# Performance work log

Hardware: AMD Instinct MI355X
Metric: run time of the kernel (lower is better)

The kernel has to match this reference:

```python
import jax, jax.numpy as jnp
from jax import lax
import numpy as np

V, H, D, B, W = 256, 512, 2, 256, 256  # vector_size, hidden_size, depth, batch, window_size


def setup_inputs() -> dict:
    key = jax.random.key(0)
    ks = jax.random.split(key, 13)
    scale = 0.04  # ~ 1/sqrt(hidden)
    names = ["w_ih_ltr", "w_hh_ltr", "b_ih_ltr", "b_hh_ltr", "w_fc_ltr", "b_fc_ltr",
             "w_ih_rtl", "w_hh_rtl", "b_ih_rtl", "b_hh_rtl", "w_fc_rtl", "b_fc_rtl"]
    shapes = [(D, 4 * H, V), (D, 4 * H, H), (D, 4 * H), (D, 4 * H), (D, V, H), (D, V)] * 2
    inp = {"x": jax.random.normal(ks[0], (B, W, V), dtype=jnp.float32)}
    for i, (n, s) in enumerate(zip(names, shapes)):
        inp[n] = jax.random.normal(ks[i + 1], s, dtype=jnp.float32) * scale
    return inp


def _lstm_cell(x, h, c, wih, whh, bih, bhh):
    # PyTorch gate order: i, f, g, o
    g = x @ wih.T + bih + h @ whh.T + bhh
    i, f, gg, o = jnp.split(g, 4, axis=-1)
    c = jax.nn.sigmoid(f) * c + jax.nn.sigmoid(i) * jnp.tanh(gg)
    h = jax.nn.sigmoid(o) * jnp.tanh(c)
    return h, c


def _run_dir(xs, wih, whh, bih, bhh, wfc, bfc):
    # xs: (T, B, V); depth LSTM(1-step)+FC blocks with persistent (h,c) per depth
    depth = wih.shape[0]
    h0 = jnp.zeros((depth, xs.shape[1], whh.shape[-1]), xs.dtype)

    def step(carry, x):
        h, c = carry
        v = x
        hs, cs = [], []
        for j in range(depth):  # small fixed depth loop
            hj, cj = _lstm_cell(v, h[j], c[j], wih[j], whh[j], bih[j], bhh[j])
            v = hj @ wfc[j].T + bfc[j]
            hs.append(hj)
            cs.append(cj)
        return (jnp.stack(hs), jnp.stack(cs)), v

    _, ys = lax.scan(step, (h0, h0), xs)
    return ys  # (T, B, V)


def reference(x, w_ih_ltr, w_hh_ltr, b_ih_ltr, b_hh_ltr, w_fc_ltr, b_fc_ltr,
              w_ih_rtl, w_hh_rtl, b_ih_rtl, b_hh_rtl, w_fc_rtl, b_fc_rtl):
    Wlen = x.shape[1]
    xs_f = jnp.swapaxes(x[:, :Wlen - 1, :], 0, 1)        # steps i = 0 .. W-2
    xs_b = jnp.swapaxes(x[:, Wlen - 1:0:-1, :], 0, 1)    # steps -(i+1) = W-1 .. 1
    ys_f = _run_dir(xs_f, w_ih_ltr, w_hh_ltr, b_ih_ltr, b_hh_ltr, w_fc_ltr, b_fc_ltr)
    ys_b = _run_dir(xs_b, w_ih_rtl, w_hh_rtl, b_ih_rtl, b_hh_rtl, w_fc_rtl, b_fc_rtl)
    # torch.stack(output, dim=1): forward outputs then backward outputs -> (B, 2*(W-1), V)
    return jnp.swapaxes(jnp.concatenate([ys_f, ys_b], axis=0), 0, 1)
```

## Files before the change

### kernel.cpp

```cpp
#include <hip/hip_runtime.h>
#include <hip/hip_bf16.h>

using bf16   = __bf16;
using bf16x8 = __attribute__((ext_vector_type(8))) __bf16;
using f32x4  = __attribute__((ext_vector_type(4))) float;
using u32x4  = __attribute__((ext_vector_type(4))) unsigned int;

#define TSTEPS 255
#define UNITE  512
#define HPAR   (16*16*512)
#define WA_UNITS_DIR (128*24)
#define WB_UNITS_DIR (128*32)
#define WC_UNITS_DIR (16*16)

#define MFMA(acc, a, b) acc = __builtin_amdgcn_mfma_f32_16x16x32_bf16((a), (b), (acc), 0, 0, 0)

__device__ __forceinline__ float sigmoidf_(float x) { return 1.f / (1.f + __expf(-x)); }
__device__ __forceinline__ float tanhf_(float x) {
    float e = __expf(-2.f * fabsf(x));
    float t = (1.f - e) / (1.f + e);
    return copysignf(t, x);
}

__device__ __forceinline__ void storeh_coh(bf16* ph, bf16* pl,
                                           unsigned short vh, unsigned short vl) {
    asm volatile(
        "global_store_short %0, %2, off sc0 sc1\n\t"
        "global_store_short %1, %3, off sc0 sc1"
        :: "v"(ph), "v"(pl), "v"(vh), "v"(vl)
        : "memory");
}

__device__ __forceinline__ void stage32k_512(const bf16* gh, const bf16* gl,
                                             bf16* lds, int tid) {
    u32x4 a0, a1, b0, b1;
    const bf16* p0 = gh + tid * 8;
    const bf16* p1 = p0 + 4096;
    const bf16* q0 = gl + tid * 8;
    const bf16* q1 = q0 + 4096;
    asm volatile(
        "global_load_dwordx4 %0, %4, off sc0 sc1\n\t"
        "global_load_dwordx4 %1, %5, off sc0 sc1\n\t"
        "global_load_dwordx4 %2, %6, off sc0 sc1\n\t"
        "global_load_dwordx4 %3, %7, off sc0 sc1\n\t"
        "s_waitcnt vmcnt(0)"
        : "=&v"(a0), "=&v"(a1), "=&v"(b0), "=&v"(b1)
        : "v"(p0), "v"(p1), "v"(q0), "v"(q1)
        : "memory");
    *(u32x4*)(lds + tid * 8)               = a0;
    *(u32x4*)(lds + tid * 8 + 4096)        = a1;
    *(u32x4*)(lds + 8192 + tid * 8)        = b0;
    *(u32x4*)(lds + 8192 + tid * 8 + 4096) = b1;
}

__device__ __forceinline__ void split_store8(const float* __restrict__ src,
                                             bf16* __restrict__ dh, bf16* __restrict__ dl) {
    float f[8];
    *(float4*)f       = *(const float4*)src;
    *(float4*)(f + 4) = *(const float4*)(src + 4);
    bf16x8 oh, ol;
    #pragma unroll
    for (int j = 0; j < 8; ++j) { bf16 h = (bf16)f[j]; oh[j] = h; ol[j] = (bf16)(f[j] - (float)h); }
    *(bf16x8*)dh = oh; *(bf16x8*)dl = ol;
}

__device__ __forceinline__ void gbarrier(unsigned* __restrict__ flags, int bid, unsigned epoch) {
    asm volatile("s_waitcnt vmcnt(0)" ::: "memory");
    __syncthreads();
    if (threadIdx.x == 0)
        asm volatile("global_store_dword %0, %1, off sc0 sc1"
                     :: "v"(&flags[bid]), "v"(epoch) : "memory");
    if (threadIdx.x < 64) {
        const int l = threadIdx.x;
        for (;;) {
            unsigned f0 = __hip_atomic_load(&flags[l],       __ATOMIC_RELAXED, __HIP_MEMORY_SCOPE_AGENT);
            unsigned f1 = __hip_atomic_load(&flags[l + 64],  __ATOMIC_RELAXED, __HIP_MEMORY_SCOPE_AGENT);
            unsigned f2 = __hip_atomic_load(&flags[l + 128], __ATOMIC_RELAXED, __HIP_MEMORY_SCOPE_AGENT);
            unsigned f3 = __hip_atomic_load(&flags[l + 192], __ATOMIC_RELAXED, __HIP_MEMORY_SCOPE_AGENT);
            if (__all(f0 >= epoch && f1 >= epoch && f2 >= epoch && f3 >= epoch)) break;
            __builtin_amdgcn_s_sleep(1);
        }
    }
    __syncthreads();
}


__global__ void k_pack_wa(const float* __restrict__ wihL, const float* __restrict__ whhL,
                          const float* __restrict__ wihR, const float* __restrict__ whhR,
                          bf16* __restrict__ wah, bf16* __restrict__ wal) {
    int gid = blockIdx.x * 256 + threadIdx.x;
    int lane = gid & 63, u = gid >> 6;
    int kb = u % 24; int tn = (u / 24) & 127; int dir = u / 3072;
    int r = lane & 15, q = lane >> 4;
    int n = tn * 16 + r, k = kb * 32 + q * 8;
    const float* wih = dir ? wihR : wihL;
    const float* whh = dir ? whhR : whhL;
    const float* src = (k < 256) ? (wih + (size_t)n * 256 + k)
                                 : (whh + (size_t)n * 512 + (k - 256));
    split_store8(src, wah + (size_t)u * UNITE + lane * 8, wal + (size_t)u * UNITE + lane * 8);
}

__global__ void k_wcomb(const float* __restrict__ wihL, const float* __restrict__ wfcL,
                        const float* __restrict__ wihR, const float* __restrict__ wfcR,
                        float* __restrict__ wcf) {
    size_t gid = (size_t)blockIdx.x * 256 + threadIdx.x;
    int k = gid & 511; int n = (gid >> 9) & 2047; int dir = (int)(gid >> 20);
    const float* wih1 = (dir ? wihR : wihL) + (size_t)2048 * 256;
    const float* wfc0 = (dir ? wfcR : wfcL);
    float s = 0.f;
    #pragma unroll 8
    for (int v = 0; v < 256; ++v)
        s = fmaf(wih1[(size_t)n * 256 + v], wfc0[(size_t)v * 512 + k], s);
    wcf[gid] = s;
}

__global__ void k_pack_wb(const float* __restrict__ whhL, const float* __restrict__ whhR,
                          const float* __restrict__ wcf,
                          bf16* __restrict__ wbh, bf16* __restrict__ wbl) {
    int gid = blockIdx.x * 256 + threadIdx.x;
    int lane = gid & 63, u = gid >> 6;
    int kb = u & 31, tn = (u >> 5) & 127, dir = u >> 12;
    int r = lane & 15, q = lane >> 4;
    int n = tn * 16 + r, k = kb * 32 + q * 8;
    const float* src;
    if (k < 512) {
        src = wcf + ((size_t)dir * 2048 + n) * 512 + k;
    } else {
        const float* whh1 = (dir ? whhR : whhL) + (size_t)2048 * 512;
        src = whh1 + (size_t)n * 512 + (k - 512);
    }
    split_store8(src, wbh + (size_t)u * UNITE + lane * 8, wbl + (size_t)u * UNITE + lane * 8);
}

__global__ void k_pack_wc(const float* __restrict__ wfcL, const float* __restrict__ wfcR,
                          bf16* __restrict__ wch, bf16* __restrict__ wcl) {
    int gid = blockIdx.x * 256 + threadIdx.x;
    int lane = gid & 63, u = gid >> 6;
    int kb = u & 15, tn = (u >> 4) & 15, dir = u >> 8;
    int r = lane & 15, q = lane >> 4;
    int n = tn * 16 + r, k = kb * 32 + q * 8;
    const float* wfc1 = (dir ? wfcR : wfcL) + (size_t)256 * 512;
    split_store8(wfc1 + (size_t)n * 512 + k,
                 wch + (size_t)u * UNITE + lane * 8, wcl + (size_t)u * UNITE + lane * 8);
}

__global__ void k_bias(const float* __restrict__ bihL, const float* __restrict__ bhhL,
                       const float* __restrict__ bfcL, const float* __restrict__ wihL,
                       const float* __restrict__ bihR, const float* __restrict__ bhhR,
                       const float* __restrict__ bfcR, const float* __restrict__ wihR,
                       float* __restrict__ ba, float* __restrict__ bb, float* __restrict__ bc) {
    int gid = blockIdx.x * 256 + threadIdx.x;
    int n = gid & 2047, dir = gid >> 11;
    const float* bih = dir ? bihR : bihL;
    const float* bhh = dir ? bhhR : bhhL;
    const float* bfc = dir ? bfcR : bfcL;
    const float* wih1 = (dir ? wihR : wihL) + (size_t)2048 * 256;
    ba[dir * 2048 + n] = bih[n] + bhh[n];
    float s = bih[2048 + n] + bhh[2048 + n];
    #pragma unroll 8
    for (int v = 0; v < 256; ++v)
        s = fmaf(bfc[v], wih1[(size_t)n * 256 + v], s);
    bb[dir * 2048 + n] = s;
    if (n < 256) bc[dir * 256 + n] = bfc[256 + n];
}

__global__ __launch_bounds__(512) void bilstm_main(
    const float* __restrict__ x,
    const bf16* __restrict__ wah, const bf16* __restrict__ wal,
    const bf16* __restrict__ wbh, const bf16* __restrict__ wbl,
    const bf16* __restrict__ wch, const bf16* __restrict__ wcl,
    bf16* __restrict__ h0pk, bf16* __restrict__ h1pk,
    const float* __restrict__ ba, const float* __restrict__ bb,
    const float* __restrict__ bc, float* __restrict__ out,
    unsigned* __restrict__ flags)
{
    const int bid  = blockIdx.x;
    const int nslc = bid & 7;
    const int bq   = (bid >> 3) & 15;
    const int dir  = bid >> 7;
    const int tid  = threadIdx.x;
    const int wv   = tid >> 6;
    const int wq   = wv & 3;
    const int kg   = wv >> 2;
    const int lane = tid & 63;
    const int r = lane & 15, q = lane >> 4;

    __shared__ __align__(16) bf16 h0s[16384];
    __shared__ __align__(16) bf16 h1s[16384];
    __shared__ __align__(16) float gred[4][4][64][4];
    __shared__ __align__(16) float yred[2][64][4];

    const bf16* WAh = wah + (size_t)dir * WA_UNITS_DIR * UNITE;
    const bf16* WAl = wal + (size_t)dir * WA_UNITS_DIR * UNITE;
    const bf16* WBh = wbh + (size_t)dir * WB_UNITS_DIR * UNITE;
    const bf16* WBl = wbl + (size_t)dir * WB_UNITS_DIR * UNITE;
    const bf16* WCh = wch + (size_t)dir * WC_UNITS_DIR * UNITE;
    const bf16* WCl = wcl + (size_t)dir * WC_UNITS_DIR * UNITE;
    bf16* H0 = h0pk + (size_t)dir * 4 * HPAR;
    bf16* H1 = h1pk + (size_t)dir * 4 * HPAR;
    const float* BA = ba + dir * 2048;
    const float* BB = bb + dir * 2048;
    const float* BC = bc + dir * 256;

    const int nbase = nslc * 4 + wq;
    const int col   = nslc * 64 + wq * 16 + r;
    const float bia0 = BA[col], bia1 = BA[512 + col], bia2 = BA[1024 + col], bia3 = BA[1536 + col];
    const float bib0 = BB[col], bib1 = BB[512 + col], bib2 = BB[1024 + col], bib3 = BB[1536 + col];

    const int hunit  = bq * 16 + nslc * 2 + (wq >> 1);
    const int hw_off = ((wq & 1) * 2 + (r >> 3)) * 128 + q * 32 + (r & 7);

    const int tn  = nslc * 2 + (wq & 1);
    const float byc = BC[tn * 16 + r];

    f32x4 c0 = {0.f, 0.f, 0.f, 0.f}, c1 = {0.f, 0.f, 0.f, 0.f};
    unsigned epoch = 0;

    #pragma unroll
    for (int k2 = 0; k2 < 4; ++k2) *(u32x4*)(h0s + tid * 8 + k2 * 4096) = (u32x4){0, 0, 0, 0};
    __syncthreads();

    for (int t = 0; t <= TSTEPS; ++t) {
        const int pw = t & 1, pr = pw ^ 1;
        stage32k_512(H1 + (size_t)pr * 2 * HPAR + (size_t)bq * 8192,
                     H1 + (size_t)pr * 2 * HPAR + HPAR + (size_t)bq * 8192, h1s, tid);
        f32x4 acc[4] = {{0,0,0,0},{0,0,0,0},{0,0,0,0},{0,0,0,0}};
        if (t < TSTEPS) {
            if (kg == 0) {
                const int pos = dir ? (255 - t) : t;
                const float* xp = x + ((size_t)(bq * 16 + r) * 256 + pos) * 256 + q * 8;
                #pragma unroll
                for (int kb = 0; kb < 8; ++kb) {
                    float xf[8];
                    *(float4*)xf       = *(const float4*)(xp + kb * 32);
                    *(float4*)(xf + 4) = *(const float4*)(xp + kb * 32 + 4);
                    bf16x8 axh, axl;
                    #pragma unroll
                    for (int j = 0; j < 8; ++j) { bf16 h = (bf16)xf[j]; axh[j] = h; axl[j] = (bf16)(xf[j] - (float)h); }
                    #pragma unroll
                    for (int g = 0; g < 4; ++g) {
                        const size_t wu = ((size_t)((g * 32 + nbase) * 24 + kb)) * UNITE + lane * 8;
                        bf16x8 bh = *(const bf16x8*)(WAh + wu);
                        bf16x8 bl = *(const bf16x8*)(WAl + wu);
                        MFMA(acc[g], axh, bh); MFMA(acc[g], axh, bl); MFMA(acc[g], axl, bh);
                    }
                }
                #pragma unroll
                for (int hk = 0; hk < 4; ++hk) {
                    bf16x8 ah = *(const bf16x8*)(h0s + hk * 512 + lane * 8);
                    bf16x8 al = *(const bf16x8*)(h0s + 8192 + hk * 512 + lane * 8);
                    #pragma unroll
                    for (int g = 0; g < 4; ++g) {
                        const size_t wu = ((size_t)((g * 32 + nbase) * 24 + 8 + hk)) * UNITE + lane * 8;
                        bf16x8 bh = *(const bf16x8*)(WAh + wu);
                        bf16x8 bl = *(const bf16x8*)(WAl + wu);
                        MFMA(acc[g], ah, bh); MFMA(acc[g], ah, bl); MFMA(acc[g], al, bh);
                    }
                }
            } else {
                #pragma unroll
                for (int hk = 4; hk < 16; ++hk) {
                    bf16x8 ah = *(const bf16x8*)(h0s + hk * 512 + lane * 8);
                    bf16x8 al = *(const bf16x8*)(h0s + 8192 + hk * 512 + lane * 8);
                    #pragma unroll
                    for (int g = 0; g < 4; ++g) {
                        const size_t wu = ((size_t)((g * 32 + nbase) * 24 + 8 + hk)) * UNITE + lane * 8;
                        bf16x8 bh = *(const bf16x8*)(WAh + wu);
                        bf16x8 bl = *(const bf16x8*)(WAl + wu);
                        MFMA(acc[g], ah, bh); MFMA(acc[g], ah, bl); MFMA(acc[g], al, bh);
                    }
                }
                #pragma unroll
                for (int g = 0; g < 4; ++g) *(f32x4*)&gred[wq][g][lane][0] = acc[g];
            }
        }
        __syncthreads();
        if (t < TSTEPS && kg == 0) {
            bf16* WH = H0 + (size_t)pw * 2 * HPAR + (size_t)hunit * 512 + hw_off;
            bf16* WL = WH + HPAR;
            #pragma unroll
            for (int i = 0; i < 4; ++i) {
                float gi = sigmoidf_(acc[0][i] + gred[wq][0][lane][i] + bia0);
                float gf = sigmoidf_(acc[1][i] + gred[wq][1][lane][i] + bia1);
                float gg = tanhf_   (acc[2][i] + gred[wq][2][lane][i] + bia2);
                float go = sigmoidf_(acc[3][i] + gred[wq][3][lane][i] + bia3);
                float cc = gf * c0[i] + gi * gg;
                c0[i] = cc;
                float hv = go * tanhf_(cc);
                bf16 hh = (bf16)hv;
                bf16 hl = (bf16)(hv - (float)hh);
                storeh_coh(WH + i * 8, WL + i * 8,
                           __builtin_bit_cast(unsigned short, hh),
                           __builtin_bit_cast(unsigned short, hl));
            }
        }
        f32x4 accy = {0, 0, 0, 0};
        if (t >= 1 && kg == 1) {
            const int kb0 = (wq >> 1) * 8;
            #pragma unroll
            for (int kk = 0; kk < 8; ++kk) {
                const int kb = kb0 + kk;
                bf16x8 ah = *(const bf16x8*)(h1s + kb * 512 + lane * 8);
                bf16x8 al = *(const bf16x8*)(h1s + 8192 + kb * 512 + lane * 8);
                const size_t wu = ((size_t)(tn * 16 + kb)) * UNITE + lane * 8;
                bf16x8 bh = *(const bf16x8*)(WCh + wu);
                bf16x8 bl = *(const bf16x8*)(WCl + wu);
                MFMA(accy, ah, bh); MFMA(accy, ah, bl); MFMA(accy, al, bh);
            }
            if (wq >= 2) *(f32x4*)&yred[wq & 1][lane][0] = accy;
        }
        __syncthreads();
        if (t >= 1 && kg == 1 && wq < 2) {
            const int tout = dir ? (255 + (t - 1)) : (t - 1);
            #pragma unroll
            for (int i = 0; i < 4; ++i)
                out[((size_t)(bq * 16 + 4 * q + i) * 510 + tout) * 256 + tn * 16 + r]
                    = accy[i] + yred[wq][lane][i] + byc;
        }
        ++epoch; gbarrier(flags, bid, epoch);
        if (t < TSTEPS) {
            stage32k_512(H0 + (size_t)pw * 2 * HPAR + (size_t)bq * 8192,
                         H0 + (size_t)pw * 2 * HPAR + HPAR + (size_t)bq * 8192, h0s, tid);
            __syncthreads();
            f32x4 accb[4] = {{0,0,0,0},{0,0,0,0},{0,0,0,0},{0,0,0,0}};
            if (kg == 0) {
                #pragma unroll
                for (int hk = 0; hk < 16; ++hk) {
                    bf16x8 ah = *(const bf16x8*)(h0s + hk * 512 + lane * 8);
                    bf16x8 al = *(const bf16x8*)(h0s + 8192 + hk * 512 + lane * 8);
                    #pragma unroll
                    for (int g = 0; g < 4; ++g) {
                        const size_t wu = ((size_t)((g * 32 + nbase) * 32 + hk)) * UNITE + lane * 8;
                        bf16x8 bh = *(const bf16x8*)(WBh + wu);
                        bf16x8 bl = *(const bf16x8*)(WBl + wu);
                        MFMA(accb[g], ah, bh); MFMA(accb[g], ah, bl); MFMA(accb[g], al, bh);
                    }
                }
            } else {
                #pragma unroll
                for (int hk = 0; hk < 16; ++hk) {
                    bf16x8 ah = *(const bf16x8*)(h1s + hk * 512 + lane * 8);
                    bf16x8 al = *(const bf16x8*)(h1s + 8192 + hk * 512 + lane * 8);
                    #pragma unroll
                    for (int g = 0; g < 4; ++g) {
                        const size_t wu = ((size_t)((g * 32 + nbase) * 32 + 16 + hk)) * UNITE + lane * 8;
                        bf16x8 bh = *(const bf16x8*)(WBh + wu);
                        bf16x8 bl = *(const bf16x8*)(WBl + wu);
                        MFMA(accb[g], ah, bh); MFMA(accb[g], ah, bl); MFMA(accb[g], al, bh);
                    }
                }
                #pragma unroll
                for (int g = 0; g < 4; ++g) *(f32x4*)&gred[wq][g][lane][0] = accb[g];
            }
            __syncthreads();
            if (kg == 0) {
                bf16* WH = H1 + (size_t)pw * 2 * HPAR + (size_t)hunit * 512 + hw_off;
                bf16* WL = WH + HPAR;
                #pragma unroll
                for (int i = 0; i < 4; ++i) {
                    float gi = sigmoidf_(accb[0][i] + gred[wq][0][lane][i] + bib0);
                    float gf = sigmoidf_(accb[1][i] + gred[wq][1][lane][i] + bib1);
                    float gg = tanhf_   (accb[2][i] + gred[wq][2][lane][i] + bib2);
                    float go = sigmoidf_(accb[3][i] + gred[wq][3][lane][i] + bib3);
                    float cc = gf * c1[i] + gi * gg;
                    c1[i] = cc;
                    float hv = go * tanhf_(cc);
                    bf16 hh = (bf16)hv;
                    bf16 hl = (bf16)(hv - (float)hh);
                    storeh_coh(WH + i * 8, WL + i * 8,
                               __builtin_bit_cast(unsigned short, hh),
                               __builtin_bit_cast(unsigned short, hl));
                }
            }
        }
        ++epoch; gbarrier(flags, bid, epoch);
    }
}

extern "C" void kernel_launch(void* const* d_in, const int* in_sizes, int n_in,
                              void* d_out, int out_size, void* d_ws, size_t ws_size,
                              hipStream_t stream) {
    (void)in_sizes; (void)n_in; (void)ws_size;
    const float* x    = (const float*)d_in[0];
    const float* wihL = (const float*)d_in[1];
    const float* whhL = (const float*)d_in[2];
    const float* bihL = (const float*)d_in[3];
    const float* bhhL = (const float*)d_in[4];
    const float* wfcL = (const float*)d_in[5];
    const float* bfcL = (const float*)d_in[6];
    const float* wihR = (const float*)d_in[7];
    const float* whhR = (const float*)d_in[8];
    const float* bihR = (const float*)d_in[9];
    const float* bhhR = (const float*)d_in[10];
    const float* wfcR = (const float*)d_in[11];
    const float* bfcR = (const float*)d_in[12];

    char* ws = (char*)d_ws;
    size_t off = 0;
    auto take = [&](size_t bytes) -> char* {
        off = (off + 255) & ~(size_t)255;
        char* p = ws + off;
        off += bytes;
        return p;
    };
    bf16*     WAH = (bf16*)take((size_t)2 * WA_UNITS_DIR * 1024);
    bf16*     WAL = (bf16*)take((size_t)2 * WA_UNITS_DIR * 1024);
    bf16*     WBH = (bf16*)take((size_t)2 * WB_UNITS_DIR * 1024);
    bf16*     WBL = (bf16*)take((size_t)2 * WB_UNITS_DIR * 1024);
    bf16*     WCH = (bf16*)take((size_t)2 * WC_UNITS_DIR * 1024);
    bf16*     WCL = (bf16*)take((size_t)2 * WC_UNITS_DIR * 1024);
    bf16*     H0  = (bf16*)take((size_t)8 * HPAR * 2);
    bf16*     H1  = (bf16*)take((size_t)8 * HPAR * 2);
    float*    WCF = (float*)take((size_t)2 * 2048 * 512 * 4);
    float*    BA  = (float*)take((size_t)2 * 2048 * 4);
    float*    BB  = (float*)take((size_t)2 * 2048 * 4);
    float*    BC  = (float*)take((size_t)2 * 256 * 4);
    unsigned* FLG = (unsigned*)take((size_t)256 * 4);

    hipMemsetAsync(H0, 0, (size_t)8 * HPAR * 2, stream);
    hipMemsetAsync(H1, 0, (size_t)8 * HPAR * 2, stream);
    hipMemsetAsync(FLG, 0, (size_t)256 * 4, stream);
    hipMemsetAsync(d_out, 0, (size_t)out_size * 4, stream);

    k_pack_wa<<<1536, 256, 0, stream>>>(wihL, whhL, wihR, whhR, WAH, WAL);
    k_wcomb  <<<8192, 256, 0, stream>>>(wihL, wfcL, wihR, wfcR, WCF);
    k_pack_wb<<<2048, 256, 0, stream>>>(whhL, whhR, WCF, WBH, WBL);
    k_pack_wc<<<128,  256, 0, stream>>>(wfcL, wfcR, WCH, WCL);
    k_bias   <<<16,   256, 0, stream>>>(bihL, bhhL, bfcL, wihL, bihR, bhhR, bfcR, wihR, BA, BB, BC);

    bilstm_main<<<256, 512, 0, stream>>>(x, WAH, WAL, WBH, WBL, WCH, WCL,
                                         H0, H1, BA, BB, BC, (float*)d_out, FLG);
}
```

Before: 28.55 ms.

## Stream LSTM gate weights through double-buffered LDS with async global-to-LDS loads

Replaces direct per-lane global loads of the layer-0 and layer-1 gate weights with asynchronous global_load_lds copies into a per-wave double-buffered LDS staging area, prefetching the next chunk while MFMAs consume the current one. It also rebalances the layer-0 K split evenly across the two wave groups (12 chunks each, with x pre-converted to bf16 pairs in registers) and sets launch_bounds to 2 blocks per CU. The goal is to hide global-memory latency on the weight stream inside the serial recurrent step. In exchange it uses more LDS and more registers for the x fragments, and relies on hand-placed vmcnt waits.

```diff
diff --git a/kernel.cpp b/kernel.cpp
--- a/kernel.cpp
+++ b/kernel.cpp
@@ -21,6 +21,14 @@
     float t = (1.f - e) / (1.f + e);
     return copysignf(t, x);
 }
+
+typedef const __attribute__((address_space(1))) void g1cv;
+typedef __attribute__((address_space(3))) void l3v;
+__device__ __forceinline__ void gll16(const void* g, void* l) {
+    __builtin_amdgcn_global_load_lds((g1cv*)g, (l3v*)l, 16, 0, 0);
+}
+#define WAITVM4 asm volatile("s_waitcnt vmcnt(4)" ::: "memory")
+#define WAITVM0 asm volatile("s_waitcnt vmcnt(0)" ::: "memory")
 
 __device__ __forceinline__ void storeh_coh(bf16* ph, bf16* pl,
                                            unsigned short vh, unsigned short vl) {
@@ -164,7 +172,7 @@
     if (n < 256) bc[dir * 256 + n] = bfc[256 + n];
 }
 
-__global__ __launch_bounds__(512) void bilstm_main(
+__global__ __launch_bounds__(512, 2) void bilstm_main(
     const float* __restrict__ x,
     const bf16* __restrict__ wah, const bf16* __restrict__ wal,
     const bf16* __restrict__ wbh, const bf16* __restrict__ wbl,
@@ -187,6 +195,7 @@
 
     __shared__ __align__(16) bf16 h0s[16384];
     __shared__ __align__(16) bf16 h1s[16384];
+    __shared__ __align__(16) bf16 wbuf[2][8][4][512];
     __shared__ __align__(16) float gred[4][4][64][4];
     __shared__ __align__(16) float yred[2][64][4];
 
@@ -213,6 +222,28 @@
     const int tn  = nslc * 2 + (wq & 1);
     const float byc = BC[tn * 16 + r];
 
+#define ISSUE_CHUNK(Wh, Wl, STRIDE, KB, C) do {                                          \
+    const int gh_ = ((C) & 1) * 2;                                                       \
+    const int bf_ = (C) & 1;                                                             \
+    const size_t u0_ = ((size_t)((gh_ * 32 + nbase) * (STRIDE) + (KB))) * UNITE + (size_t)lane * 8; \
+    const size_t u1_ = ((size_t)(((gh_ + 1) * 32 + nbase) * (STRIDE) + (KB))) * UNITE + (size_t)lane * 8; \
+    gll16((const void*)((Wh) + u0_), (void*)&wbuf[bf_][wv][0][0]);                       \
+    gll16((const void*)((Wl) + u0_), (void*)&wbuf[bf_][wv][1][0]);                       \
+    gll16((const void*)((Wh) + u1_), (void*)&wbuf[bf_][wv][2][0]);                       \
+    gll16((const void*)((Wl) + u1_), (void*)&wbuf[bf_][wv][3][0]);                       \
+} while (0)
+
+#define COMPUTE_CHUNK(AH, AL, C) do {                                                    \
+    const int gh_ = ((C) & 1) * 2;                                                       \
+    const int bf_ = (C) & 1;                                                             \
+    bf16x8 bh0_ = *(const bf16x8*)&wbuf[bf_][wv][0][lane * 8];                           \
+    bf16x8 bl0_ = *(const bf16x8*)&wbuf[bf_][wv][1][lane * 8];                           \
+    bf16x8 bh1_ = *(const bf16x8*)&wbuf[bf_][wv][2][lane * 8];                           \
+    bf16x8 bl1_ = *(const bf16x8*)&wbuf[bf_][wv][3][lane * 8];                           \
+    MFMA(acc[gh_], (AH), bh0_); MFMA(acc[gh_], (AH), bl0_); MFMA(acc[gh_], (AL), bh0_);  \
+    MFMA(acc[gh_ + 1], (AH), bh1_); MFMA(acc[gh_ + 1], (AH), bl1_); MFMA(acc[gh_ + 1], (AL), bh1_); \
+} while (0)
+
     f32x4 c0 = {0.f, 0.f, 0.f, 0.f}, c1 = {0.f, 0.f, 0.f, 0.f};
     unsigned epoch = 0;
 
@@ -224,74 +255,65 @@
         const int pw = t & 1, pr = pw ^ 1;
         stage32k_512(H1 + (size_t)pr * 2 * HPAR + (size_t)bq * 8192,
                      H1 + (size_t)pr * 2 * HPAR + HPAR + (size_t)bq * 8192, h1s, tid);
-        f32x4 acc[4] = {{0,0,0,0},{0,0,0,0},{0,0,0,0},{0,0,0,0}};
-        if (t < TSTEPS) {
-            if (kg == 0) {
-                const int pos = dir ? (255 - t) : t;
-                const float* xp = x + ((size_t)(bq * 16 + r) * 256 + pos) * 256 + q * 8;
-                #pragma unroll
-                for (int kb = 0; kb < 8; ++kb) {
-                    float xf[8];
-                    *(float4*)xf       = *(const float4*)(xp + kb * 32);
-                    *(float4*)(xf + 4) = *(const float4*)(xp + kb * 32 + 4);
-                    bf16x8 axh, axl;
+        {
+            f32x4 acc[4] = {{0,0,0,0},{0,0,0,0},{0,0,0,0},{0,0,0,0}};
+            if (t < TSTEPS) {
+                bf16x8 axh[8], axl[8];
+                if (kg == 0) {
+                    const int pos = dir ? (255 - t) : t;
+                    const float* xp = x + ((size_t)(bq * 16 + r) * 256 + pos) * 256 + q * 8;
                     #pragma unroll
-                    for (int j = 0; j < 8; ++j) { bf16 h = (bf16)xf[j]; axh[j] = h; axl[j] = (bf16)(xf[j] - (float)h); }
-                    #pragma unroll
-                    for (int g = 0; g < 4; ++g) {
-                        const size_t wu = ((size_t)((g * 32 + nbase) * 24 + kb)) * UNITE + lane * 8;
-                        bf16x8 bh = *(const bf16x8*)(WAh + wu);
-                        bf16x8 bl = *(const bf16x8*)(WAl + wu);
-                        MFMA(acc[g], axh, bh); MFMA(acc[g], axh, bl); MFMA(acc[g], axl, bh);
+                    for (int kb = 0; kb < 8; ++kb) {
+                        float xf[8];
+                        *(float4*)xf       = *(const float4*)(xp + kb * 32);
+                        *(float4*)(xf + 4) = *(const float4*)(xp + kb * 32 + 4);
+                        #pragma unroll
+                        for (int j = 0; j < 8; ++j) {
+                            bf16 h = (bf16)xf[j];
+                            axh[kb][j] = h; axl[kb][j] = (bf16)(xf[j] - (float)h);
+                        }
                     }
                 }
+                const int kbb = kg * 12;
+                ISSUE_CHUNK(WAh, WAl, 24, kbb, 0);
                 #pragma unroll
-                for (int hk = 0; hk < 4; ++hk) {
-                    bf16x8 ah = *(const bf16x8*)(h0s + hk * 512 + lane * 8);
-                    bf16x8 al = *(const bf16x8*)(h0s + 8192 + hk * 512 + lane * 8);
+                for (int c = 0; c < 24; ++c) {
+                    if (c + 1 < 24) { ISSUE_CHUNK(WAh, WAl, 24, kbb + ((c + 1) >> 1), c + 1); WAITVM4; }
+                    else            { WAITVM0; }
+                    const int idx = c >> 1;
+                    bf16x8 ah, al;
+                    if (kg == 0 && idx < 8) { ah = axh[idx]; al = axl[idx]; }
+                    else {
+                        const int hk = kbb + idx - 8;
+                        ah = *(const bf16x8*)(h0s + hk * 512 + lane * 8);
+                        al = *(const bf16x8*)(h0s + 8192 + hk * 512 + lane * 8);
+                    }
+                    COMPUTE_CHUNK(ah, al, c);
+                }
+                if (kg == 1) {
                     #pragma unroll
-                    for (int g = 0; g < 4; ++g) {
-                        const size_t wu = ((size_t)((g * 32 + nbase) * 24 + 8 + hk)) * UNITE + lane * 8;
-                        bf16x8 bh = *(const bf16x8*)(WAh + wu);
-                        bf16x8 bl = *(const bf16x8*)(WAl + wu);
-                        MFMA(acc[g], ah, bh); MFMA(acc[g], ah, bl); MFMA(acc[g], al, bh);
-                    }
+                    for (int g = 0; g < 4; ++g) *(f32x4*)&gred[wq][g][lane][0] = acc[g];
                 }
-            } else {
+            }
+            __syncthreads();
+            if (t < TSTEPS && kg == 0) {
+                bf16* WH = H0 + (size_t)pw * 2 * HPAR + (size_t)hunit * 512 + hw_off;
+                bf16* WL = WH + HPAR;
                 #pragma unroll
-                for (int hk = 4; hk < 16; ++hk) {
-                    bf16x8 ah = *(const bf16x8*)(h0s + hk * 512 + lane * 8);
-                    bf16x8 al = *(const bf16x8*)(h0s + 8192 + hk * 512 + lane * 8);
-                    #pragma unroll
-                    for (int g = 0; g < 4; ++g) {
-                        const size_t wu = ((size_t)((g * 32 + nbase) * 24 + 8 + hk)) * UNITE + lane * 8;
-                        bf16x8 bh = *(const bf16x8*)(WAh + wu);
-                        bf16x8 bl = *(const bf16x8*)(WAl + wu);
-                        MFMA(acc[g], ah, bh); MFMA(acc[g], ah, bl); MFMA(acc[g], al, bh);
-                    }
+                for (int i = 0; i < 4; ++i) {
+                    float gi = sigmoidf_(acc[0][i] + gred[wq][0][lane][i] + bia0);
+                    float gf = sigmoidf_(acc[1][i] + gred[wq][1][lane][i] + bia1);
+                    float gg = tanhf_   (acc[2][i] + gred[wq][2][lane][i] + bia2);
+                    float go = sigmoidf_(acc[3][i] + gred[wq][3][lane][i] + bia3);
+                    float cc = gf * c0[i] + gi * gg;
+                    c0[i] = cc;
+                    float hv = go * tanhf_(cc);
+                    bf16 hh = (bf16)hv;
+                    bf16 hl = (bf16)(hv - (float)hh);
+                    storeh_coh(WH + i * 8, WL + i * 8,
+                               __builtin_bit_cast(unsigned short, hh),
+                               __builtin_bit_cast(unsigned short, hl));
                 }
-                #pragma unroll
-                for (int g = 0; g < 4; ++g) *(f32x4*)&gred[wq][g][lane][0] = acc[g];
-            }
-        }
-        __syncthreads();
-        if (t < TSTEPS && kg == 0) {
-            bf16* WH = H0 + (size_t)pw * 2 * HPAR + (size_t)hunit * 512 + hw_off;
-            bf16* WL = WH + HPAR;
-            #pragma unroll
-            for (int i = 0; i < 4; ++i) {
-                float gi = sigmoidf_(acc[0][i] + gred[wq][0][lane][i] + bia0);
-                float gf = sigmoidf_(acc[1][i] + gred[wq][1][lane][i] + bia1);
-                float gg = tanhf_   (acc[2][i] + gred[wq][2][lane][i] + bia2);
-                float go = sigmoidf_(acc[3][i] + gred[wq][3][lane][i] + bia3);
-                float cc = gf * c0[i] + gi * gg;
-                c0[i] = cc;
-                float hv = go * tanhf_(cc);
-                bf16 hh = (bf16)hv;
-                bf16 hl = (bf16)(hv - (float)hh);
-                storeh_coh(WH + i * 8, WL + i * 8,
-                           __builtin_bit_cast(unsigned short, hh),
-                           __builtin_bit_cast(unsigned short, hl));
             }
         }
         f32x4 accy = {0, 0, 0, 0};
@@ -305,7 +327,9 @@
                 const size_t wu = ((size_t)(tn * 16 + kb)) * UNITE + lane * 8;
                 bf16x8 bh = *(const bf16x8*)(WCh + wu);
                 bf16x8 bl = *(const bf16x8*)(WCl + wu);
-                MFMA(accy, ah, bh); MFMA(accy, ah, bl); MFMA(accy, al, bh);
+                f32x4 t0 = accy;
+                MFMA(t0, ah, bh); MFMA(t0, ah, bl); MFMA(t0, al, bh);
+                accy = t0;
             }
             if (wq >= 2) *(f32x4*)&yred[wq & 1][lane][0] = accy;
         }
@@ -322,35 +346,22 @@
             stage32k_512(H0 + (size_t)pw * 2 * HPAR + (size_t)bq * 8192,
                          H0 + (size_t)pw * 2 * HPAR + HPAR + (size_t)bq * 8192, h0s, tid);
             __syncthreads();
-            f32x4 accb[4] = {{0,0,0,0},{0,0,0,0},{0,0,0,0},{0,0,0,0}};
-            if (kg == 0) {
+            f32x4 acc[4] = {{0,0,0,0},{0,0,0,0},{0,0,0,0},{0,0,0,0}};
+            const int kbb = kg * 16;
+            ISSUE_CHUNK(WBh, WBl, 32, kbb, 0);
+            #pragma unroll
+            for (int c = 0; c < 32; ++c) {
+                if (c + 1 < 32) { ISSUE_CHUNK(WBh, WBl, 32, kbb + ((c + 1) >> 1), c + 1); WAITVM4; }
+                else            { WAITVM0; }
+                const int idx = c >> 1;
+                const bf16* hs = (kg == 0) ? h0s : h1s;
+                bf16x8 ah = *(const bf16x8*)(hs + idx * 512 + lane * 8);
+                bf16x8 al = *(const bf16x8*)(hs + 8192 + idx * 512 + lane * 8);
+                COMPUTE_CHUNK(ah, al, c);
+            }
+            if (kg == 1) {
                 #pragma unroll
-                for (int hk = 0; hk < 16; ++hk) {
-                    bf16x8 ah = *(const bf16x8*)(h0s + hk * 512 + lane * 8);
-                    bf16x8 al = *(const bf16x8*)(h0s + 8192 + hk * 512 + lane * 8);
-                    #pragma unroll
-                    for (int g = 0; g < 4; ++g) {
-                        const size_t wu = ((size_t)((g * 32 + nbase) * 32 + hk)) * UNITE + lane * 8;
-                        bf16x8 bh = *(const bf16x8*)(WBh + wu);
-                        bf16x8 bl = *(const bf16x8*)(WBl + wu);
-                        MFMA(accb[g], ah, bh); MFMA(accb[g], ah, bl); MFMA(accb[g], al, bh);
-                    }
-                }
-            } else {
-                #pragma unroll
-                for (int hk = 0; hk < 16; ++hk) {
-                    bf16x8 ah = *(const bf16x8*)(h1s + hk * 512 + lane * 8);
-                    bf16x8 al = *(const bf16x8*)(h1s + 8192 + hk * 512 + lane * 8);
-                    #pragma unroll
-                    for (int g = 0; g < 4; ++g) {
-                        const size_t wu = ((size_t)((g * 32 + nbase) * 32 + 16 + hk)) * UNITE + lane * 8;
-                        bf16x8 bh = *(const bf16x8*)(WBh + wu);
-                        bf16x8 bl = *(const bf16x8*)(WBl + wu);
-                        MFMA(accb[g], ah, bh); MFMA(accb[g], ah, bl); MFMA(accb[g], al, bh);
-                    }
-                }
-                #pragma unroll
-                for (int g = 0; g < 4; ++g) *(f32x4*)&gred[wq][g][lane][0] = accb[g];
+                for (int g = 0; g < 4; ++g) *(f32x4*)&gred[wq][g][lane][0] = acc[g];
             }
             __syncthreads();
             if (kg == 0) {
@@ -358,10 +369,10 @@
                 bf16* WL = WH + HPAR;
                 #pragma unroll
                 for (int i = 0; i < 4; ++i) {
-                    float gi = sigmoidf_(accb[0][i] + gred[wq][0][lane][i] + bib0);
-                    float gf = sigmoidf_(accb[1][i] + gred[wq][1][lane][i] + bib1);
-                    float gg = tanhf_   (accb[2][i] + gred[wq][2][lane][i] + bib2);
-                    float go = sigmoidf_(accb[3][i] + gred[wq][3][lane][i] + bib3);
+                    float gi = sigmoidf_(acc[0][i] + gred[wq][0][lane][i] + bib0);
+                    float gf = sigmoidf_(acc[1][i] + gred[wq][1][lane][i] + bib1);
+                    float gg = tanhf_   (acc[2][i] + gred[wq][2][lane][i] + bib2);
+                    float go = sigmoidf_(acc[3][i] + gred[wq][3][lane][i] + bib3);
                     float cc = gf * c1[i] + gi * gg;
                     c1[i] = cc;
                     float hv = go * tanhf_(cc);
@@ -375,6 +386,8 @@
         }
         ++epoch; gbarrier(flags, bid, epoch);
     }
+#undef ISSUE_CHUNK
+#undef COMPUTE_CHUNK
 }
 
 extern "C" void kernel_launch(void* const* d_in, const int* in_sizes, int n_in,
```

New measurement: 29.11 ms. Within noise of the previous version (+2.0%).
